# Kernel tuning notes

Hardware: AMD Instinct MI355X
Metric: run time of the kernel (lower is better)

Reference implementation:

```python
import jax, jax.numpy as jnp
import numpy as np

B, N, IN_DIM, SLOT_DIM, HIDDEN = 32, 4096, 256, 256, 512
NUM_SLOTS, NUM_ITERS = 8, 3
EPS_LN = 1e-5


def layernorm(x, g, b):
    m = jnp.mean(x, axis=-1, keepdims=True)
    v = jnp.var(x, axis=-1, keepdims=True)
    return (x - m) * jax.lax.rsqrt(v + EPS_LN) * g + b


def setup_inputs() -> dict:
    key = jax.random.key(0)
    ks = jax.random.split(key, 16)
    s = 0.02
    return {
        "inputs": jax.random.normal(ks[0], (B, N, IN_DIM), jnp.float32),
        "init_noise": jax.random.normal(ks[1], (B, NUM_SLOTS, SLOT_DIM), jnp.float32),
        "mu": jax.random.normal(ks[2], (1, 1, SLOT_DIM), jnp.float32),
        "sigma_raw": jax.random.normal(ks[3], (1, 1, SLOT_DIM), jnp.float32),
        "ln_in_g": jnp.ones((IN_DIM,), jnp.float32), "ln_in_b": jnp.zeros((IN_DIM,), jnp.float32),
        "ln_s_g": jnp.ones((SLOT_DIM,), jnp.float32), "ln_s_b": jnp.zeros((SLOT_DIM,), jnp.float32),
        "ln_m_g": jnp.ones((SLOT_DIM,), jnp.float32), "ln_m_b": jnp.zeros((SLOT_DIM,), jnp.float32),
        "wq": jax.random.normal(ks[4], (SLOT_DIM, SLOT_DIM), jnp.float32) * s,
        "bq": jnp.zeros((SLOT_DIM,), jnp.float32),
        "wk": jax.random.normal(ks[5], (SLOT_DIM, IN_DIM), jnp.float32) * s,
        "bk": jnp.zeros((SLOT_DIM,), jnp.float32),
        "wv": jax.random.normal(ks[6], (SLOT_DIM, IN_DIM), jnp.float32) * s,
        "bv": jnp.zeros((SLOT_DIM,), jnp.float32),
        "w_ih": jax.random.normal(ks[7], (3 * SLOT_DIM, SLOT_DIM), jnp.float32) * s,
        "w_hh": jax.random.normal(ks[8], (3 * SLOT_DIM, SLOT_DIM), jnp.float32) * s,
        "b_ih": jnp.zeros((3 * SLOT_DIM,), jnp.float32),
        "b_hh": jnp.zeros((3 * SLOT_DIM,), jnp.float32),
        "w1": jax.random.normal(ks[9], (HIDDEN, SLOT_DIM), jnp.float32) * s,
        "b1": jnp.zeros((HIDDEN,), jnp.float32),
        "w2": jax.random.normal(ks[10], (SLOT_DIM, HIDDEN), jnp.float32) * s,
        "b2": jnp.zeros((SLOT_DIM,), jnp.float32),
    }


def gru_cell(x, h, w_ih, w_hh, b_ih, b_hh):
    # PyTorch GRUCell: gates split as (reset, update, new)
    gx = x @ w_ih.T + b_ih
    gh = h @ w_hh.T + b_hh
    xr, xz, xn = jnp.split(gx, 3, axis=-1)
    hr, hz, hn = jnp.split(gh, 3, axis=-1)
    r = jax.nn.sigmoid(xr + hr)
    z = jax.nn.sigmoid(xz + hz)
    n = jnp.tanh(xn + r * hn)
    return (1.0 - z) * n + z * h


def reference(inputs, init_noise, mu, sigma_raw, ln_in_g, ln_in_b, ln_s_g, ln_s_b,
              ln_m_g, ln_m_b, wq, bq, wk, bk, wv, bv, w_ih, w_hh, b_ih, b_hh,
              w1, b1, w2, b2):
    scale = SLOT_DIM ** (-0.5)
    x = layernorm(inputs, ln_in_g, ln_in_b)          # [B,N,Din]
    k = x @ wk.T + bk                                # [B,N,D]
    v = x @ wv.T + bv                                # [B,N,D]
    sigma = jax.nn.softplus(sigma_raw)
    slots = mu + sigma * init_noise                  # [B,S,D]
    attn = None
    for _ in range(NUM_ITERS):
        slots_prev = slots
        q = layernorm(slots, ln_s_g, ln_s_b) @ wq.T + bq      # [B,S,D]
        logits = jnp.einsum('bnd,bsd->bns', k, q) * scale     # [B,N,S]
        attn = jax.nn.softmax(logits, axis=-1) + 1e-8         # softmax over slots
        attn = attn / jnp.sum(attn, axis=1, keepdims=True)    # renorm over inputs
        updates = jnp.einsum('bnd,bns->bsd', v, attn)         # [B,S,D]
        slots = gru_cell(updates, slots_prev, w_ih, w_hh, b_ih, b_hh)
        h = jax.nn.relu(layernorm(slots, ln_m_g, ln_m_b) @ w1.T + b1)
        slots = slots + (h @ w2.T + b2)
    return slots, attn
```

## Files before the change

kernel.cpp:

```cpp
#include <hip/hip_runtime.h>
#include <hip/hip_fp16.h>
#include <cstdint>

#define DEV static __device__ __forceinline__

typedef _Float16 f16x2 __attribute__((ext_vector_type(2)));
typedef _Float16 f16x8 __attribute__((ext_vector_type(8)));
typedef float    f32x4 __attribute__((ext_vector_type(4)));

DEV float fdot2u(uint32_t a, uint32_t b, float c){
  union U { uint32_t u; f16x2 h; };
  U ua; ua.u = a; U ub; ub.u = b;
#if __has_builtin(__builtin_amdgcn_fdot2)
  return __builtin_amdgcn_fdot2(ua.h, ub.h, c, false);
#else
  return c + (float)ua.h[0]*(float)ub.h[0] + (float)ua.h[1]*(float)ub.h[1];
#endif
}

DEV float dot4(uint4 x, uint4 w, float a){
  a = fdot2u(x.x, w.x, a); a = fdot2u(x.y, w.y, a);
  a = fdot2u(x.z, w.z, a); a = fdot2u(x.w, w.w, a);
  return a;
}

DEV float wsum64(float v){
  #pragma unroll
  for (int o = 32; o; o >>= 1) v += __shfl_xor(v, o);
  return v;
}

DEV uint32_t pack2h(float a, float b){
  __half ha = __float2half(a), hb = __float2half(b);
  return (uint32_t)__half_as_ushort(ha) | ((uint32_t)__half_as_ushort(hb) << 16);
}

DEV uint32_t packsh(float v){
  float o = __shfl_xor(v, 1);
  return pack2h(v, o);
}

DEV uint4 packrow8(const float* p){
  uint4 r;
  r.x = pack2h(p[0], p[1]); r.y = pack2h(p[2], p[3]);
  r.z = pack2h(p[4], p[5]); r.w = pack2h(p[6], p[7]);
  return r;
}

DEV void gld16(const void* g, void* l){
  __builtin_amdgcn_global_load_lds(
      (const __attribute__((address_space(1))) void*)g,
      (__attribute__((address_space(3))) void*)l, 16, 0, 0);
}

__global__ __launch_bounds__(256) void k_lntr(
  const float* __restrict__ xin, const float* __restrict__ lng,
  const float* __restrict__ lnb, uint32_t* __restrict__ xhat,
  const float* __restrict__ wq, const float* __restrict__ wv,
  const float* __restrict__ wih, const float* __restrict__ whh,
  const float* __restrict__ w1, const float* __restrict__ w2,
  const float* __restrict__ wk,
  uint4* __restrict__ WQp4, uint4* __restrict__ WVp4,
  uint4* __restrict__ WIHp4, uint4* __restrict__ WHHp4,
  uint4* __restrict__ W1p4, uint4* __restrict__ W2p4,
  uint4* __restrict__ WKp4)
{
  if (blockIdx.x >= 32768){
    int u = (blockIdx.x - 32768) * 256 + threadIdx.x;
    if (u < 8192){
      int e4 = u >> 8, n = u & 255;
      WVp4[u] = packrow8(wv + n*256 + 8*e4);
    } else if (u < 32768){
      int v = u - 8192; int e4 = v / 768, n = v - e4*768;
      WIHp4[v] = packrow8(wih + n*256 + 8*e4);
    } else if (u < 57344){
      int v = u - 32768; int e4 = v / 768, n = v - e4*768;
      WHHp4[v] = packrow8(whh + n*256 + 8*e4);
    } else if (u < 73728){
      int v = u - 57344; int e4 = v >> 9, n = v & 511;
      W1p4[v] = packrow8(w1 + n*256 + 8*e4);
    } else if (u < 90112){
      int v = u - 73728; int e4 = v >> 8, n = v & 255;
      W2p4[v] = packrow8(w2 + n*512 + 8*e4);
    } else if (u < 98304){
      int v = u - 90112; int e4 = v >> 8, n = v & 255;
      WQp4[v] = packrow8(wq + n*256 + 8*e4);
    } else if (u < 106496){
      int v = u - 98304; int d4 = v >> 8, c = v & 255;
      uint4 r;
      r.x = pack2h(wk[(8*d4+0)*256 + c], wk[(8*d4+1)*256 + c]);
      r.y = pack2h(wk[(8*d4+2)*256 + c], wk[(8*d4+3)*256 + c]);
      r.z = pack2h(wk[(8*d4+4)*256 + c], wk[(8*d4+5)*256 + c]);
      r.w = pack2h(wk[(8*d4+6)*256 + c], wk[(8*d4+7)*256 + c]);
      WKp4[v] = r;
    }
    return;
  }
  int row = blockIdx.x * 4 + (threadIdx.x >> 6);
  int lane = threadIdx.x & 63;
  const float4 xv = ((const float4*)(xin + (size_t)row * 256))[lane];
  float s1 = wsum64(xv.x + xv.y + xv.z + xv.w);
  float s2 = wsum64(xv.x*xv.x + xv.y*xv.y + xv.z*xv.z + xv.w*xv.w);
  float m = s1 * (1.0f/256.0f);
  float var = s2 * (1.0f/256.0f) - m*m;
  float rstd = rsqrtf(var + 1e-5f);
  float4 gv = ((const float4*)lng)[lane];
  float4 bv = ((const float4*)lnb)[lane];
  float y0 = (xv.x - m)*rstd*gv.x + bv.x;
  float y1 = (xv.y - m)*rstd*gv.y + bv.y;
  float y2 = (xv.z - m)*rstd*gv.z + bv.z;
  float y3 = (xv.w - m)*rstd*gv.w + bv.w;
  ((uint2*)(xhat + (size_t)row * 128))[lane] = make_uint2(pack2h(y0,y1), pack2h(y2,y3));
}

template<int MODE>
__global__ __launch_bounds__(512) void k_slot(
  const float* __restrict__ noise, const float* __restrict__ mu,
  const float* __restrict__ sigraw,
  const float* S0, float* SDST,
  const float* __restrict__ UAp, const float* __restrict__ ASp,
  float* __restrict__ OUTA,
  const uint4* __restrict__ WVp4, const float* __restrict__ bv,
  const uint4* __restrict__ WIHp4, const uint4* __restrict__ WHHp4,
  const float* __restrict__ bih, const float* __restrict__ bhh,
  const float* __restrict__ lmg, const float* __restrict__ lmb,
  const uint4* __restrict__ W1p4, const float* __restrict__ b1,
  const uint4* __restrict__ W2p4, const float* __restrict__ b2,
  const float* __restrict__ lsg, const float* __restrict__ lsb,
  const uint4* __restrict__ WQp4, const float* __restrict__ bq,
  const uint4* __restrict__ WKp4, const float* __restrict__ bk,
  uint32_t* __restrict__ QTH, float* __restrict__ CV)
{
  __shared__ float gx[768], gh[768];
  __shared__ float part[512];
  __shared__ uint4 hs4[32], un4[32], us4[32], sln4[32], q4[32];
  __shared__ uint4 hb4[64];
  __shared__ float redA[8], redB[8];
  __shared__ float asb[8];

  const int t = threadIdx.x;
  const int h = t >> 8;
  const int c = t & 255;
  const int lane = t & 63;
  const int w8 = t >> 6;
  const int r = blockIdx.x;
  const int b = r >> 3, s = r & 7;

  float snv = 0.f, spv = 0.f;

  if (MODE == 0){
    if (t < 256){
      float x = sigraw[c];
      float sp = (x > 20.0f) ? x : log1pf(__expf(x));
      snv = mu[c] + sp * noise[r*256 + c];
      SDST[r*256 + c] = snv;
    }
  } else {
    if (MODE == 2){
      if (lane < 16){
        float v = ASp[lane*256 + b*8 + w8];
        v += __shfl_xor(v, 1); v += __shfl_xor(v, 2);
        v += __shfl_xor(v, 4); v += __shfl_xor(v, 8);
        if (lane == 0) asb[w8] = v;
      }
    } else {
      if (w8 == 0){
        float v = (lane < 16) ? ASp[lane*256 + r] : 0.f;
        v += __shfl_xor(v, 1); v += __shfl_xor(v, 2);
        v += __shfl_xor(v, 4); v += __shfl_xor(v, 8);
        if (lane == 0) redA[0] = v;
      }
    }
    __syncthreads();
    const float asum_r = (MODE == 2) ? asb[s] : redA[0];
    const float ainv = 1.0f / asum_r;
    float hv = 0.f;
    if (t < 256){
      hv = S0[r*256 + c];
      float us = 0.f;
      #pragma unroll
      for (int ch = 0; ch < 16; ++ch) us += UAp[ch*65536 + r*256 + c];
      float unv = us * ainv;
      uint32_t ph = packsh(hv), pu = packsh(unv);
      if (!(c & 1)){
        ((uint32_t*)hs4)[c>>1] = ph;
        ((uint32_t*)un4)[c>>1] = pu;
      }
    }
    __syncthreads();

    {
      float a = 0.f;
      #pragma unroll 8
      for (int e4 = h*16; e4 < h*16 + 16; ++e4)
        a = dot4(un4[e4], WVp4[e4*256 + c], a);
      part[t] = a;
    }
    __syncthreads();
    if (t < 256){
      float us = part[t] + part[t + 256] + bv[c];
      uint32_t p = packsh(us);
      if (!(c & 1)) ((uint32_t*)us4)[c>>1] = p;
    }
    __syncthreads();

    {
      const uint4* IN4 = h ? hs4 : us4;
      const uint4* WP = h ? WHHp4 : WIHp4;
      float a0 = 0.f, a1 = 0.f, a2 = 0.f;
      #pragma unroll 8
      for (int e4 = 0; e4 < 32; ++e4){
        uint4 x = IN4[e4];
        a0 = dot4(x, WP[e4*768 + c], a0);
        a1 = dot4(x, WP[e4*768 + 256 + c], a1);
        a2 = dot4(x, WP[e4*768 + 512 + c], a2);
      }
      float* OUT = h ? gh : gx;
      OUT[c] = a0; OUT[256 + c] = a1; OUT[512 + c] = a2;
    }
    __syncthreads();

    if (t < 256){
      float xr = gx[c]     + bih[c];
      float xz = gx[256+c] + bih[256+c];
      float xn = gx[512+c] + bih[512+c];
      float hr = gh[c]     + bhh[c];
      float hz = gh[256+c] + bhh[256+c];
      float hn = gh[512+c] + bhh[512+c];
      float rg = 1.f/(1.f + __expf(-(xr + hr)));
      float zg = 1.f/(1.f + __expf(-(xz + hz)));
      float ng = tanhf(xn + rg*hn);
      spv = (1.f - zg)*ng + zg*hv;
      float a = wsum64(spv), bs = wsum64(spv*spv);
      if (lane == 0){ redA[w8] = a; redB[w8] = bs; }
    }
    __syncthreads();
    {
      float s1 = redA[0]+redA[1]+redA[2]+redA[3];
      float s2 = redB[0]+redB[1]+redB[2]+redB[3];
      float m = s1*(1.f/256.f), var = s2*(1.f/256.f) - m*m;
      float rstd = rsqrtf(var + 1e-5f);
      if (t < 256){
        float slv = (spv - m)*rstd*lmg[c] + lmb[c];
        uint32_t p = packsh(slv);
        if (!(c & 1)) ((uint32_t*)sln4)[c>>1] = p;
      }
    }
    __syncthreads();

    {
      float a = 0.f;
      #pragma unroll 8
      for (int e4 = 0; e4 < 32; ++e4)
        a = dot4(sln4[e4], W1p4[e4*512 + t], a);
      float hval = fmaxf(a + b1[t], 0.f);
      float o = __shfl_xor(hval, 1);
      if (!(t & 1)) ((uint32_t*)hb4)[t>>1] = pack2h(hval, o);
    }
    __syncthreads();

    {
      float a = 0.f;
      #pragma unroll 8
      for (int e4 = h*32; e4 < h*32 + 32; ++e4)
        a = dot4(hb4[e4], W2p4[e4*256 + c], a);
      part[t] = a;
    }
    __syncthreads();
    if (t < 256){
      snv = spv + part[t] + part[t + 256] + b2[c];
      SDST[r*256 + c] = snv;
    }
  }

  if (MODE != 2){
    if (t < 256){
      float a = wsum64(snv), bs = wsum64(snv*snv);
      if (lane == 0){ redA[w8] = a; redB[w8] = bs; }
    }
    __syncthreads();
    {
      float s1 = redA[0]+redA[1]+redA[2]+redA[3];
      float s2 = redB[0]+redB[1]+redB[2]+redB[3];
      float m = s1*(1.f/256.f), var = s2*(1.f/256.f) - m*m;
      float rstd = rsqrtf(var + 1e-5f);
      if (t < 256){
        float slv = (snv - m)*rstd*lsg[c] + lsb[c];
        uint32_t p = packsh(slv);
        if (!(c & 1)) ((uint32_t*)sln4)[c>>1] = p;
      }
    }
    __syncthreads();

    {
      float a = 0.f;
      #pragma unroll 8
      for (int e4 = h*16; e4 < h*16 + 16; ++e4)
        a = dot4(sln4[e4], WQp4[e4*256 + c], a);
      part[t] = a;
    }
    __syncthreads();
    if (t < 256){
      float qv = part[t] + part[t + 256] + bq[c];
      float p = wsum64(bk[c] * qv);
      if (lane == 0) redA[w8] = p;
      uint32_t pk = packsh(qv);
      if (!(c & 1)) ((uint32_t*)q4)[c>>1] = pk;
    }
    __syncthreads();
    {
      float cv = redA[0]+redA[1]+redA[2]+redA[3];
      if (t == 0) CV[r] = cv;
    }

    {
      float a = 0.f;
      #pragma unroll 8
      for (int e4 = h*16; e4 < h*16 + 16; ++e4)
        a = dot4(q4[e4], WKp4[e4*256 + c], a);
      part[t] = a;
    }
    __syncthreads();
    if (t < 256){
      float qtv = part[t] + part[t + 256];
      uint32_t p = packsh(qtv);
      if (!(c & 1)) QTH[b*1024 + (c>>1)*8 + s] = p;
    }
  } else if (s == 0){
    float inv[8];
    #pragma unroll
    for (int j = 0; j < 8; ++j) inv[j] = 1.0f / asb[j];
    float4* ap = (float4*)(OUTA + (size_t)b * 32768);
    #pragma unroll 4
    for (int i = t; i < 8192; i += 512){
      float4 v = ap[i];
      int h4 = (i & 1) * 4;
      v.x *= inv[h4+0]; v.y *= inv[h4+1]; v.z *= inv[h4+2]; v.w *= inv[h4+3];
      ap[i] = v;
    }
  }
}

template<bool LAST>
__global__ __launch_bounds__(256) void k_attn(
  const uint32_t* __restrict__ xhat,
  const uint32_t* __restrict__ qtpk, const float* __restrict__ cvec,
  float* __restrict__ UAp, float* __restrict__ ASp,
  float* __restrict__ attn_out)
{
  __shared__ __align__(16) uint32_t xs[2][8192];
  __shared__ uint32_t qs[1024];
  __shared__ float attn_lds[64][16];
  __shared__ float as_red[4][8];
  float* up_lds = (float*)&xs[0][0];

  const int b = blockIdx.y, chunk = blockIdx.x;
  const int t = threadIdx.x;
  const int l = t & 63, w = t >> 6;
  const int g = l >> 4, sl = l & 15;

  const size_t base = (size_t)b*4096 + (size_t)chunk*256;

  for (int i = t; i < 1024; i += 256) qs[i] = qtpk[b*1024 + i];

  auto stage = [&](int st){
    uint32_t* dst = &xs[st & 1][0];
    const size_t gr0 = base + (size_t)st*64;
    #pragma unroll
    for (int i = 0; i < 8; ++i){
      int n  = w*8 + i;
      int rl = 2*n + (l >> 5);
      int ql = (l & 31) ^ (rl & 7);
      gld16(xhat + (gr0 + rl)*128 + ql*4, dst + n*256);
    }
  };

  stage(0);
  __syncthreads();

  uint4 bq[8];
  #pragma unroll
  for (int kk = 0; kk < 8; ++kk){
    if (sl < 8){
      uint4 v;
      v.x = qs[(16*kk + 4*g + 0)*8 + sl];
      v.y = qs[(16*kk + 4*g + 1)*8 + sl];
      v.z = qs[(16*kk + 4*g + 2)*8 + sl];
      v.w = qs[(16*kk + 4*g + 3)*8 + sl];
      bq[kk] = v;
    } else bq[kk] = make_uint4(0u,0u,0u,0u);
  }
  const float cv = (sl < 8) ? cvec[b*8 + sl] : 0.f;

  float up[8][4];
  #pragma unroll
  for (int s = 0; s < 8; ++s){ up[s][0]=0.f; up[s][1]=0.f; up[s][2]=0.f; up[s][3]=0.f; }
  float asl_acc = 0.f;

  for (int st = 0; st < 4; ++st){
    if (st) __syncthreads();
    if (st < 3) stage(st + 1);
    const uint32_t* xb = &xs[st & 1][0];
    const int L0 = 16*w;

    f32x4 acc; acc[0]=0.f; acc[1]=0.f; acc[2]=0.f; acc[3]=0.f;
    const int rowA = L0 + sl;
    #pragma unroll
    for (int kk = 0; kk < 8; ++kk){
      uint4 av = *(const uint4*)(xb + rowA*128 + (((4*kk + g) ^ (rowA & 7)) << 2));
      union { uint4 u; f16x8 h; } A, B;
      A.u = av; B.u = bq[kk];
      acc = __builtin_amdgcn_mfma_f32_16x16x32_f16(A.h, B.h, acc, 0, 0, 0);
    }

    #pragma unroll
    for (int reg = 0; reg < 4; ++reg){
      float d = (acc[reg] + cv) * 0.0625f;
      float m = d;
      m = fmaxf(m, __shfl_xor(m, 1));
      m = fmaxf(m, __shfl_xor(m, 2));
      m = fmaxf(m, __shfl_xor(m, 4));
      float e = __expf(d - m);
      float ssum = e;
      ssum += __shfl_xor(ssum, 1);
      ssum += __shfl_xor(ssum, 2);
      ssum += __shfl_xor(ssum, 4);
      float a = e / ssum + 1e-8f;
      asl_acc += a;
      attn_lds[L0 + 4*g + reg][sl] = a;
    }

    #pragma unroll 4
    for (int rr = 0; rr < 16; ++rr){
      const int row = L0 + rr;
      const uint32_t* xp = xb + row*128 + ((((l>>1) ^ (row & 7)) << 2) | ((l & 1) << 1));
      uint2 xv = *(const uint2*)xp;
      float x0 = __half2float(__ushort_as_half((unsigned short)(xv.x & 0xffff)));
      float x1 = __half2float(__ushort_as_half((unsigned short)(xv.x >> 16)));
      float x2 = __half2float(__ushort_as_half((unsigned short)(xv.y & 0xffff)));
      float x3 = __half2float(__ushort_as_half((unsigned short)(xv.y >> 16)));
      const float4 a0 = *(const float4*)&attn_lds[row][0];
      const float4 a1 = *(const float4*)&attn_lds[row][4];
      float as8[8] = {a0.x, a0.y, a0.z, a0.w, a1.x, a1.y, a1.z, a1.w};
      #pragma unroll
      for (int s = 0; s < 8; ++s){
        up[s][0] += as8[s]*x0; up[s][1] += as8[s]*x1;
        up[s][2] += as8[s]*x2; up[s][3] += as8[s]*x3;
      }
    }

    if (LAST){
      __syncthreads();
      int row = t >> 2, s0 = (t & 3)*2;
      float2 v = *(const float2*)&attn_lds[row][s0];
      *(float2*)(attn_out + (base + (size_t)st*64 + row)*8 + s0) = v;
    }
  }

  {
    float v = asl_acc;
    v += __shfl_xor(v, 16);
    v += __shfl_xor(v, 32);
    if (l < 8) as_red[w][l] = v;
  }

  __syncthreads();
  #pragma unroll
  for (int ww = 0; ww < 4; ++ww){
    if (w == ww){
      #pragma unroll
      for (int s = 0; s < 8; ++s){
        float4* dst = (float4*)&up_lds[s*256 + l*4];
        float4 v = make_float4(up[s][0], up[s][1], up[s][2], up[s][3]);
        if (ww){ float4 o = *dst; v.x += o.x; v.y += o.y; v.z += o.z; v.w += o.w; }
        *dst = v;
      }
    }
    __syncthreads();
  }
  #pragma unroll
  for (int s = 0; s < 8; ++s)
    UAp[(size_t)chunk*65536 + (size_t)(b*8 + s)*256 + t] = up_lds[s*256 + t];
  if (t < 8)
    ASp[chunk*256 + b*8 + t] = as_red[0][t] + as_red[1][t] + as_red[2][t] + as_red[3][t];
}

extern "C" void kernel_launch(void* const* d_in, const int* in_sizes, int n_in,
                              void* d_out, int out_size, void* d_ws, size_t ws_size,
                              hipStream_t stream) {
  const float* inputs = (const float*)d_in[0];
  const float* noise  = (const float*)d_in[1];
  const float* mu     = (const float*)d_in[2];
  const float* sigraw = (const float*)d_in[3];
  const float* lng    = (const float*)d_in[4];
  const float* lnb    = (const float*)d_in[5];
  const float* lsg    = (const float*)d_in[6];
  const float* lsb    = (const float*)d_in[7];
  const float* lmg    = (const float*)d_in[8];
  const float* lmb    = (const float*)d_in[9];
  const float* wq     = (const float*)d_in[10];
  const float* bq     = (const float*)d_in[11];
  const float* wk     = (const float*)d_in[12];
  const float* bk     = (const float*)d_in[13];
  const float* wv     = (const float*)d_in[14];
  const float* bv     = (const float*)d_in[15];
  const float* wih    = (const float*)d_in[16];
  const float* whh    = (const float*)d_in[17];
  const float* bih    = (const float*)d_in[18];
  const float* bhh    = (const float*)d_in[19];
  const float* w1     = (const float*)d_in[20];
  const float* b1     = (const float*)d_in[21];
  const float* w2     = (const float*)d_in[22];
  const float* b2     = (const float*)d_in[23];
  float* out = (float*)d_out;

  char* w = (char*)d_ws;
  size_t o = 0;
  uint32_t* XH = (uint32_t*)w;  o += 67108864;
  uint32_t* QT = (uint32_t*)(w + o); o += 131072;
  float* CV  = (float*)(w + o); o += 1024;
  float* S0  = (float*)(w + o); o += 262144;
  uint4* WQp = (uint4*)(w + o); o += 131072;
  uint4* WVp = (uint4*)(w + o); o += 131072;
  uint4* WIHp= (uint4*)(w + o); o += 393216;
  uint4* WHHp= (uint4*)(w + o); o += 393216;
  uint4* W1p = (uint4*)(w + o); o += 262144;
  uint4* W2p = (uint4*)(w + o); o += 262144;
  uint4* WKp = (uint4*)(w + o); o += 131072;
  float* UAp = (float*)(w + o); o += 4194304;
  float* ASp = (float*)(w + o); o += 16384;

  float* OUTA = out + 65536;

  k_lntr<<<33184, 256, 0, stream>>>(inputs, lng, lnb, XH,
                                    wq, wv, wih, whh, w1, w2, wk,
                                    WQp, WVp, WIHp, WHHp, W1p, W2p, WKp);
  k_slot<0><<<256, 512, 0, stream>>>(noise, mu, sigraw, S0, S0, UAp, ASp, OUTA,
      WVp, bv, WIHp, WHHp, bih, bhh, lmg, lmb, W1p, b1, W2p, b2,
      lsg, lsb, WQp, bq, WKp, bk, QT, CV);

  dim3 ga(16, 32);
  for (int it = 0; it < 3; ++it){
    if (it == 2) k_attn<true ><<<ga, 256, 0, stream>>>(XH, QT, CV, UAp, ASp, OUTA);
    else         k_attn<false><<<ga, 256, 0, stream>>>(XH, QT, CV, UAp, ASp, OUTA);
    if (it < 2)
      k_slot<1><<<256, 512, 0, stream>>>(noise, mu, sigraw, S0, S0, UAp, ASp, OUTA,
          WVp, bv, WIHp, WHHp, bih, bhh, lmg, lmb, W1p, b1, W2p, b2,
          lsg, lsb, WQp, bq, WKp, bk, QT, CV);
    else
      k_slot<2><<<256, 512, 0, stream>>>(noise, mu, sigraw, S0, out, UAp, ASp, OUTA,
          WVp, bv, WIHp, WHHp, bih, bhh, lmg, lmb, W1p, b1, W2p, b2,
          lsg, lsb, WQp, bq, WKp, bk, QT, CV);
  }
}
```

Baseline: 377.3 us.

## Fold initial slot/query setup into prep kernel; single-buffer attention LDS staging

Removes the separate k_slot<0> launch by adding 256 extra blocks to the layernorm/weight-packing kernel. These blocks compute the initial slots, their layernorm, q, q·bk and the transposed q·Wk product in fp32 straight from the raw weights. In k_attn the double-buffered input staging becomes single-buffered, with a sync before and after each stage load, and a separate LDS array for the update reduction. This saves a launch and lowers LDS use, but load latency is no longer overlapped with MFMA compute in the attention loop. Also, the new q-projection blocks read fp32 Wq and Wk uncoalesced per thread.

Result: slower. 411.9 us (+9.2%).

```diff
diff --git a/kernel.cpp b/kernel.cpp
--- a/kernel.cpp
+++ b/kernel.cpp
@@ -63,10 +63,59 @@
   uint4* __restrict__ WQp4, uint4* __restrict__ WVp4,
   uint4* __restrict__ WIHp4, uint4* __restrict__ WHHp4,
   uint4* __restrict__ W1p4, uint4* __restrict__ W2p4,
-  uint4* __restrict__ WKp4)
+  uint4* __restrict__ WKp4,
+  const float* __restrict__ noise, const float* __restrict__ mu,
+  const float* __restrict__ sigraw,
+  const float* __restrict__ lsg, const float* __restrict__ lsb,
+  const float* __restrict__ bq, const float* __restrict__ bk,
+  float* __restrict__ S0, uint32_t* __restrict__ QT, float* __restrict__ CV)
 {
+  const int t = threadIdx.x;
+  if (blockIdx.x >= 33184){
+    __shared__ float sln[256], qsh[256];
+    __shared__ float redA[4], redB[4];
+    const int r = blockIdx.x - 33184;
+    const int b = r >> 3, s = r & 7;
+    const int lane = t & 63, w4 = t >> 6;
+    float x = sigraw[t];
+    float sp = (x > 20.0f) ? x : log1pf(__expf(x));
+    float snv = mu[t] + sp * noise[r*256 + t];
+    S0[r*256 + t] = snv;
+    float a = wsum64(snv), bs = wsum64(snv*snv);
+    if (lane == 0){ redA[w4] = a; redB[w4] = bs; }
+    __syncthreads();
+    {
+      float s1 = redA[0]+redA[1]+redA[2]+redA[3];
+      float s2 = redB[0]+redB[1]+redB[2]+redB[3];
+      float m = s1*(1.f/256.f), var = s2*(1.f/256.f) - m*m;
+      float rstd = rsqrtf(var + 1e-5f);
+      sln[t] = (snv - m)*rstd*lsg[t] + lsb[t];
+    }
+    __syncthreads();
+    float qa = 0.f;
+    const float4* wr = (const float4*)(wq + t*256);
+    #pragma unroll 8
+    for (int k4 = 0; k4 < 64; ++k4){
+      float4 wv4 = wr[k4];
+      const float* sl = sln + k4*4;
+      qa += wv4.x*sl[0] + wv4.y*sl[1] + wv4.z*sl[2] + wv4.w*sl[3];
+    }
+    float qv = qa + bq[t];
+    float pcv = wsum64(bk[t] * qv);
+    if (lane == 0) redA[w4] = pcv;
+    qsh[t] = qv;
+    __syncthreads();
+    if (t == 0) CV[r] = redA[0]+redA[1]+redA[2]+redA[3];
+    float qta = 0.f;
+    #pragma unroll 8
+    for (int d = 0; d < 256; ++d)
+      qta += qsh[d] * wk[d*256 + t];
+    uint32_t p = packsh(qta);
+    if (!(t & 1)) QT[b*1024 + (t>>1)*8 + s] = p;
+    return;
+  }
   if (blockIdx.x >= 32768){
-    int u = (blockIdx.x - 32768) * 256 + threadIdx.x;
+    int u = (blockIdx.x - 32768) * 256 + t;
     if (u < 8192){
       int e4 = u >> 8, n = u & 255;
       WVp4[u] = packrow8(wv + n*256 + 8*e4);
@@ -96,8 +145,8 @@
     }
     return;
   }
-  int row = blockIdx.x * 4 + (threadIdx.x >> 6);
-  int lane = threadIdx.x & 63;
+  int row = blockIdx.x * 4 + (t >> 6);
+  int lane = t & 63;
   const float4 xv = ((const float4*)(xin + (size_t)row * 256))[lane];
   float s1 = wsum64(xv.x + xv.y + xv.z + xv.w);
   float s2 = wsum64(xv.x*xv.x + xv.y*xv.y + xv.z*xv.z + xv.w*xv.w);
@@ -115,8 +164,6 @@
 
 template<int MODE>
 __global__ __launch_bounds__(512) void k_slot(
-  const float* __restrict__ noise, const float* __restrict__ mu,
-  const float* __restrict__ sigraw,
   const float* S0, float* SDST,
   const float* __restrict__ UAp, const float* __restrict__ ASp,
   float* __restrict__ OUTA,
@@ -148,129 +195,120 @@
 
   float snv = 0.f, spv = 0.f;
 
-  if (MODE == 0){
+  if (MODE == 2){
+    if (lane < 16){
+      float v = ASp[lane*256 + b*8 + w8];
+      v += __shfl_xor(v, 1); v += __shfl_xor(v, 2);
+      v += __shfl_xor(v, 4); v += __shfl_xor(v, 8);
+      if (lane == 0) asb[w8] = v;
+    }
+  } else {
+    if (w8 == 0){
+      float v = (lane < 16) ? ASp[lane*256 + r] : 0.f;
+      v += __shfl_xor(v, 1); v += __shfl_xor(v, 2);
+      v += __shfl_xor(v, 4); v += __shfl_xor(v, 8);
+      if (lane == 0) redA[0] = v;
+    }
+  }
+  __syncthreads();
+  const float asum_r = (MODE == 2) ? asb[s] : redA[0];
+  const float ainv = 1.0f / asum_r;
+  float hv = 0.f;
+  if (t < 256){
+    hv = S0[r*256 + c];
+    float us = 0.f;
+    #pragma unroll
+    for (int ch = 0; ch < 16; ++ch) us += UAp[ch*65536 + r*256 + c];
+    float unv = us * ainv;
+    uint32_t ph = packsh(hv), pu = packsh(unv);
+    if (!(c & 1)){
+      ((uint32_t*)hs4)[c>>1] = ph;
+      ((uint32_t*)un4)[c>>1] = pu;
+    }
+  }
+  __syncthreads();
+
+  {
+    float a = 0.f;
+    #pragma unroll 8
+    for (int e4 = h*16; e4 < h*16 + 16; ++e4)
+      a = dot4(un4[e4], WVp4[e4*256 + c], a);
+    part[t] = a;
+  }
+  __syncthreads();
+  if (t < 256){
+    float us = part[t] + part[t + 256] + bv[c];
+    uint32_t p = packsh(us);
+    if (!(c & 1)) ((uint32_t*)us4)[c>>1] = p;
+  }
+  __syncthreads();
+
+  {
+    const uint4* IN4 = h ? hs4 : us4;
+    const uint4* WP = h ? WHHp4 : WIHp4;
+    float a0 = 0.f, a1 = 0.f, a2 = 0.f;
+    #pragma unroll 8
+    for (int e4 = 0; e4 < 32; ++e4){
+      uint4 x = IN4[e4];
+      a0 = dot4(x, WP[e4*768 + c], a0);
+      a1 = dot4(x, WP[e4*768 + 256 + c], a1);
+      a2 = dot4(x, WP[e4*768 + 512 + c], a2);
+    }
+    float* OUT = h ? gh : gx;
+    OUT[c] = a0; OUT[256 + c] = a1; OUT[512 + c] = a2;
+  }
+  __syncthreads();
+
+  if (t < 256){
+    float xr = gx[c]     + bih[c];
+    float xz = gx[256+c] + bih[256+c];
+    float xn = gx[512+c] + bih[512+c];
+    float hr = gh[c]     + bhh[c];
+    float hz = gh[256+c] + bhh[256+c];
+    float hn = gh[512+c] + bhh[512+c];
+    float rg = 1.f/(1.f + __expf(-(xr + hr)));
+    float zg = 1.f/(1.f + __expf(-(xz + hz)));
+    float ng = tanhf(xn + rg*hn);
+    spv = (1.f - zg)*ng + zg*hv;
+    float a = wsum64(spv), bs = wsum64(spv*spv);
+    if (lane == 0){ redA[w8] = a; redB[w8] = bs; }
+  }
+  __syncthreads();
+  {
+    float s1 = redA[0]+redA[1]+redA[2]+redA[3];
+    float s2 = redB[0]+redB[1]+redB[2]+redB[3];
+    float m = s1*(1.f/256.f), var = s2*(1.f/256.f) - m*m;
+    float rstd = rsqrtf(var + 1e-5f);
     if (t < 256){
-      float x = sigraw[c];
-      float sp = (x > 20.0f) ? x : log1pf(__expf(x));
-      snv = mu[c] + sp * noise[r*256 + c];
-      SDST[r*256 + c] = snv;
-    }
-  } else {
-    if (MODE == 2){
-      if (lane < 16){
-        float v = ASp[lane*256 + b*8 + w8];
-        v += __shfl_xor(v, 1); v += __shfl_xor(v, 2);
-        v += __shfl_xor(v, 4); v += __shfl_xor(v, 8);
-        if (lane == 0) asb[w8] = v;
-      }
-    } else {
-      if (w8 == 0){
-        float v = (lane < 16) ? ASp[lane*256 + r] : 0.f;
-        v += __shfl_xor(v, 1); v += __shfl_xor(v, 2);
-        v += __shfl_xor(v, 4); v += __shfl_xor(v, 8);
-        if (lane == 0) redA[0] = v;
-      }
-    }
-    __syncthreads();
-    const float asum_r = (MODE == 2) ? asb[s] : redA[0];
-    const float ainv = 1.0f / asum_r;
-    float hv = 0.f;
-    if (t < 256){
-      hv = S0[r*256 + c];
-      float us = 0.f;
-      #pragma unroll
-      for (int ch = 0; ch < 16; ++ch) us += UAp[ch*65536 + r*256 + c];
-      float unv = us * ainv;
-      uint32_t ph = packsh(hv), pu = packsh(unv);
-      if (!(c & 1)){
-        ((uint32_t*)hs4)[c>>1] = ph;
-        ((uint32_t*)un4)[c>>1] = pu;
-      }
-    }
-    __syncthreads();
-
-    {
-      float a = 0.f;
-      #pragma unroll 8
-      for (int e4 = h*16; e4 < h*16 + 16; ++e4)
-        a = dot4(un4[e4], WVp4[e4*256 + c], a);
-      part[t] = a;
-    }
-    __syncthreads();
-    if (t < 256){
-      float us = part[t] + part[t + 256] + bv[c];
-      uint32_t p = packsh(us);
-      if (!(c & 1)) ((uint32_t*)us4)[c>>1] = p;
-    }
-    __syncthreads();
-
-    {
-      const uint4* IN4 = h ? hs4 : us4;
-      const uint4* WP = h ? WHHp4 : WIHp4;
-      float a0 = 0.f, a1 = 0.f, a2 = 0.f;
-      #pragma unroll 8
-      for (int e4 = 0; e4 < 32; ++e4){
-        uint4 x = IN4[e4];
-        a0 = dot4(x, WP[e4*768 + c], a0);
-        a1 = dot4(x, WP[e4*768 + 256 + c], a1);
-        a2 = dot4(x, WP[e4*768 + 512 + c], a2);
-      }
-      float* OUT = h ? gh : gx;
-      OUT[c] = a0; OUT[256 + c] = a1; OUT[512 + c] = a2;
-    }
-    __syncthreads();
-
-    if (t < 256){
-      float xr = gx[c]     + bih[c];
-      float xz = gx[256+c] + bih[256+c];
-      float xn = gx[512+c] + bih[512+c];
-      float hr = gh[c]     + bhh[c];
-      float hz = gh[256+c] + bhh[256+c];
-      float hn = gh[512+c] + bhh[512+c];
-      float rg = 1.f/(1.f + __expf(-(xr + hr)));
-      float zg = 1.f/(1.f + __expf(-(xz + hz)));
-      float ng = tanhf(xn + rg*hn);
-      spv = (1.f - zg)*ng + zg*hv;
-      float a = wsum64(spv), bs = wsum64(spv*spv);
-      if (lane == 0){ redA[w8] = a; redB[w8] = bs; }
-    }
-    __syncthreads();
-    {
-      float s1 = redA[0]+redA[1]+redA[2]+redA[3];
-      float s2 = redB[0]+redB[1]+redB[2]+redB[3];
-      float m = s1*(1.f/256.f), var = s2*(1.f/256.f) - m*m;
-      float rstd = rsqrtf(var + 1e-5f);
-      if (t < 256){
-        float slv = (spv - m)*rstd*lmg[c] + lmb[c];
-        uint32_t p = packsh(slv);
-        if (!(c & 1)) ((uint32_t*)sln4)[c>>1] = p;
-      }
-    }
-    __syncthreads();
-
-    {
-      float a = 0.f;
-      #pragma unroll 8
-      for (int e4 = 0; e4 < 32; ++e4)
-        a = dot4(sln4[e4], W1p4[e4*512 + t], a);
-      float hval = fmaxf(a + b1[t], 0.f);
-      float o = __shfl_xor(hval, 1);
-      if (!(t & 1)) ((uint32_t*)hb4)[t>>1] = pack2h(hval, o);
-    }
-    __syncthreads();
-
-    {
-      float a = 0.f;
-      #pragma unroll 8
-      for (int e4 = h*32; e4 < h*32 + 32; ++e4)
-        a = dot4(hb4[e4], W2p4[e4*256 + c], a);
-      part[t] = a;
-    }
-    __syncthreads();
-    if (t < 256){
-      snv = spv + part[t] + part[t + 256] + b2[c];
-      SDST[r*256 + c] = snv;
-    }
+      float slv = (spv - m)*rstd*lmg[c] + lmb[c];
+      uint32_t p = packsh(slv);
+      if (!(c & 1)) ((uint32_t*)sln4)[c>>1] = p;
+    }
+  }
+  __syncthreads();
+
+  {
+    float a = 0.f;
+    #pragma unroll 8
+    for (int e4 = 0; e4 < 32; ++e4)
+      a = dot4(sln4[e4], W1p4[e4*512 + t], a);
+    float hval = fmaxf(a + b1[t], 0.f);
+    float o = __shfl_xor(hval, 1);
+    if (!(t & 1)) ((uint32_t*)hb4)[t>>1] = pack2h(hval, o);
+  }
+  __syncthreads();
+
+  {
+    float a = 0.f;
+    #pragma unroll 8
+    for (int e4 = h*32; e4 < h*32 + 32; ++e4)
+      a = dot4(hb4[e4], W2p4[e4*256 + c], a);
+    part[t] = a;
+  }
+  __syncthreads();
+  if (t < 256){
+    snv = spv + part[t] + part[t + 256] + b2[c];
+    SDST[r*256 + c] = snv;
   }
 
   if (MODE != 2){
@@ -348,11 +386,11 @@
   float* __restrict__ UAp, float* __restrict__ ASp,
   float* __restrict__ attn_out)
 {
-  __shared__ __align__(16) uint32_t xs[2][8192];
+  __shared__ uint32_t xs[8192];
   __shared__ uint32_t qs[1024];
   __shared__ float attn_lds[64][16];
+  __shared__ float up_lds[8][256];
   __shared__ float as_red[4][8];
-  float* up_lds = (float*)&xs[0][0];
 
   const int b = blockIdx.y, chunk = blockIdx.x;
   const int t = threadIdx.x;
@@ -364,14 +402,13 @@
   for (int i = t; i < 1024; i += 256) qs[i] = qtpk[b*1024 + i];
 
   auto stage = [&](int st){
-    uint32_t* dst = &xs[st & 1][0];
     const size_t gr0 = base + (size_t)st*64;
     #pragma unroll
     for (int i = 0; i < 8; ++i){
       int n  = w*8 + i;
       int rl = 2*n + (l >> 5);
       int ql = (l & 31) ^ (rl & 7);
-      gld16(xhat + (gr0 + rl)*128 + ql*4, dst + n*256);
+      gld16(xhat + (gr0 + rl)*128 + ql*4, xs + n*256);
     }
   };
 
@@ -398,16 +435,14 @@
   float asl_acc = 0.f;
 
   for (int st = 0; st < 4; ++st){
-    if (st) __syncthreads();
-    if (st < 3) stage(st + 1);
-    const uint32_t* xb = &xs[st & 1][0];
+    if (st){ __syncthreads(); stage(st); __syncthreads(); }
     const int L0 = 16*w;
 
     f32x4 acc; acc[0]=0.f; acc[1]=0.f; acc[2]=0.f; acc[3]=0.f;
     const int rowA = L0 + sl;
     #pragma unroll
     for (int kk = 0; kk < 8; ++kk){
-      uint4 av = *(const uint4*)(xb + rowA*128 + (((4*kk + g) ^ (rowA & 7)) << 2));
+      uint4 av = *(const uint4*)(xs + rowA*128 + (((4*kk + g) ^ (rowA & 7)) << 2));
       union { uint4 u; f16x8 h; } A, B;
       A.u = av; B.u = bq[kk];
       acc = __builtin_amdgcn_mfma_f32_16x16x32_f16(A.h, B.h, acc, 0, 0, 0);
@@ -433,7 +468,7 @@
     #pragma unroll 4
     for (int rr = 0; rr < 16; ++rr){
       const int row = L0 + rr;
-      const uint32_t* xp = xb + row*128 + ((((l>>1) ^ (row & 7)) << 2) | ((l & 1) << 1));
+      const uint32_t* xp = xs + row*128 + ((((l>>1) ^ (row & 7)) << 2) | ((l & 1) << 1));
       uint2 xv = *(const uint2*)xp;
       float x0 = __half2float(__ushort_as_half((unsigned short)(xv.x & 0xffff)));
       float x1 = __half2float(__ushort_as_half((unsigned short)(xv.x >> 16)));
@@ -470,7 +505,7 @@
     if (w == ww){
       #pragma unroll
       for (int s = 0; s < 8; ++s){
-        float4* dst = (float4*)&up_lds[s*256 + l*4];
+        float4* dst = (float4*)&up_lds[s][l*4];
         float4 v = make_float4(up[s][0], up[s][1], up[s][2], up[s][3]);
         if (ww){ float4 o = *dst; v.x += o.x; v.y += o.y; v.z += o.z; v.w += o.w; }
         *dst = v;
@@ -480,7 +515,7 @@
   }
   #pragma unroll
   for (int s = 0; s < 8; ++s)
-    UAp[(size_t)chunk*65536 + (size_t)(b*8 + s)*256 + t] = up_lds[s*256 + t];
+    UAp[(size_t)chunk*65536 + (size_t)(b*8 + s)*256 + t] = up_lds[s][t];
   if (t < 8)
     ASp[chunk*256 + b*8 + t] = as_red[0][t] + as_red[1][t] + as_red[2][t] + as_red[3][t];
 }
@@ -532,23 +567,22 @@
 
   float* OUTA = out + 65536;
 
-  k_lntr<<<33184, 256, 0, stream>>>(inputs, lng, lnb, XH,
+  k_lntr<<<33440, 256, 0, stream>>>(inputs, lng, lnb, XH,
                                     wq, wv, wih, whh, w1, w2, wk,
-                                    WQp, WVp, WIHp, WHHp, W1p, W2p, WKp);
-  k_slot<0><<<256, 512, 0, stream>>>(noise, mu, sigraw, S0, S0, UAp, ASp, OUTA,
-      WVp, bv, WIHp, WHHp, bih, bhh, lmg, lmb, W1p, b1, W2p, b2,
-      lsg, lsb, WQp, bq, WKp, bk, QT, CV);
+                                    WQp, WVp, WIHp, WHHp, W1p, W2p, WKp,
+                                    noise, mu, sigraw, lsg, lsb, bq, bk,
+                                    S0, QT, CV);
 
   dim3 ga(16, 32);
   for (int it = 0; it < 3; ++it){
     if (it == 2) k_attn<true ><<<ga, 256, 0, stream>>>(XH, QT, CV, UAp, ASp, OUTA);
     else         k_attn<false><<<ga, 256, 0, stream>>>(XH, QT, CV, UAp, ASp, OUTA);
     if (it < 2)
-      k_slot<1><<<256, 512, 0, stream>>>(noise, mu, sigraw, S0, S0, UAp, ASp, OUTA,
+      k_slot<1><<<256, 512, 0, stream>>>(S0, S0, UAp, ASp, OUTA,
           WVp, bv, WIHp, WHHp, bih, bhh, lmg, lmb, W1p, b1, W2p, b2,
           lsg, lsb, WQp, bq, WKp, bk, QT, CV);
     else
-      k_slot<2><<<256, 512, 0, stream>>>(noise, mu, sigraw, S0, out, UAp, ASp, OUTA,
+      k_slot<2><<<256, 512, 0, stream>>>(S0, out, UAp, ASp, OUTA,
           WVp, bv, WIHp, WHHp, bih, bhh, lmg, lmb, W1p, b1, W2p, b2,
           lsg, lsb, WQp, bq, WKp, bk, QT, CV);
   }
```
